# Kernel optimization log

Measured on AMD Instinct MI355X. Metric: run time of the kernel, lower is better.

The kernel has to match this reference:

```python
import jax, jax.numpy as jnp
import numpy as np

N, IN_F, OUT_F, K = 256, 8192, 8320, 16
J = OUT_F - IN_F  # 128


def setup_inputs() -> dict:
    key = jax.random.key(0)
    k1, k2 = jax.random.split(key)
    tensor = jax.random.normal(k1, (N, IN_F), dtype=jnp.float32)
    T = jax.random.normal(k2, (IN_F, J, K), dtype=jnp.float32)
    return {"tensor": tensor, "T": T}


def reference(tensor, T):
    # flatten(start_dim=1) is identity for rank-2 input
    x = tensor.reshape(tensor.shape[0], -1)            # [N, IN_F]
    feats = jnp.einsum('ni,ijk->njk', x, T)            # [N, J, K]
    # pairwise L1 across batch: [N,1,J,K] - [N,J,K] -> [N,N,J,K]
    diff = jnp.abs(feats[:, None, :, :] - feats[None, :, :, :])
    l1 = jnp.sum(diff, axis=3)                         # [N, N, J]
    diversity = jnp.sum(jnp.exp(-l1), axis=1)          # [N, J]
    return jnp.concatenate((x, diversity), axis=1)     # [N, IN_F + J]
```

## Files before the change

kernel.cpp:

```cpp
#include <hip/hip_runtime.h>

typedef unsigned int  u32;
typedef unsigned short u16;

typedef __bf16 bf16x8 __attribute__((ext_vector_type(8)));
typedef float  floatx4 __attribute__((ext_vector_type(4)));

#define N_ROWS 256
#define IN_F   8192
#define OUT_F  8320
#define JDIM   128
#define KDIM   16
#define JK     2048

#define BM     256
#define BN     64
#define BK     64
#define WSTRIDE 72

typedef const __attribute__((address_space(1))) u32 gu32;
typedef __attribute__((address_space(3))) u32 su32;

__device__ __forceinline__ u16 f2bf(float f) {
    u32 u = __float_as_uint(f);
    return (u16)((u + 0x7fffu + ((u >> 16) & 1u)) >> 16);
}
__device__ __forceinline__ float bf2f(u16 h) { return __uint_as_float(((u32)h) << 16); }

__global__ __launch_bounds__(256) void prep_kernel(const float* __restrict__ X,
                                                   float* __restrict__ out,
                                                   u16* __restrict__ Xb)
{
    int t = blockIdx.x * 256 + threadIdx.x;
    float4 v = reinterpret_cast<const float4*>(X)[t];
    int row = t >> 11;
    int c4  = t & 2047;
    reinterpret_cast<float4*>(out + (size_t)row * OUT_F)[c4] = v;
    ushort4 b;
    b.x = f2bf(v.x); b.y = f2bf(v.y); b.z = f2bf(v.z); b.w = f2bf(v.w);
    reinterpret_cast<ushort4*>(Xb)[t] = b;
    if (t < 8192) {
        int r2 = t >> 5, j4 = t & 31;
        reinterpret_cast<float4*>(out + (size_t)r2 * OUT_F + IN_F)[j4] = make_float4(0.f, 0.f, 0.f, 0.f);
    }
}

__global__ __launch_bounds__(256) void gemm_kernel(const u16* __restrict__ Xb,
                                                   const float* __restrict__ W,
                                                   u16* __restrict__ slabs,
                                                   int kchunk)
{
    __shared__ u16 xs[BM * BK];
    __shared__ u16 wt[BN * WSTRIDE];

    const int tid  = threadIdx.x;
    const int lane = tid & 63;
    const int wave = tid >> 6;
    const int c0   = blockIdx.x * BN;
    const int s    = blockIdx.y;
    const int k0base = s * kchunk;

    floatx4 acc[4][4] = {};

    const int xrl = lane >> 3;
    const int xgc = (lane & 7) ^ xrl;
    const int wk  = (tid >> 4) << 2;
    const int wc  = (tid & 15) << 2;

    const float* wptr = W + (size_t)(k0base + wk) * JK + c0 + wc;

    float4 wreg[4];
    #pragma unroll
    for (int r = 0; r < 4; ++r)
        wreg[r] = *(const float4*)(wptr + (size_t)r * JK);

    const int iters = kchunk >> 6;
    for (int it = 0; it < iters; ++it) {
        const int k0 = k0base + it * BK;
        __syncthreads();

        #pragma unroll
        for (int g = 0; g < 8; ++g) {
            int rbase = wave * 64 + g * 8;
            const u16* gp = Xb + (size_t)(rbase + xrl) * IN_F + k0 + xgc * 8;
            u32* lp = (u32*)&xs[rbase * BK];
            __builtin_amdgcn_global_load_lds((gu32*)gp, (su32*)lp, 16, 0, 0);
        }

        {
            const float* wr = (const float*)wreg;
            #pragma unroll
            for (int i = 0; i < 4; ++i) {
                u32 lo = (u32)f2bf(wr[0 * 4 + i]) | ((u32)f2bf(wr[1 * 4 + i]) << 16);
                u32 hi = (u32)f2bf(wr[2 * 4 + i]) | ((u32)f2bf(wr[3 * 4 + i]) << 16);
                uint2 v; v.x = lo; v.y = hi;
                *(uint2*)&wt[(wc + i) * WSTRIDE + wk] = v;
            }
        }
        __syncthreads();

        if (it + 1 < iters) {
            const float* wn = wptr + (size_t)(it + 1) * BK * JK;
            #pragma unroll
            for (int r = 0; r < 4; ++r)
                wreg[r] = *(const float4*)(wn + (size_t)r * JK);
        }

        const int mrow = lane & 15;
        const int q    = lane >> 4;
        #pragma unroll
        for (int h = 0; h < 2; ++h) {
            bf16x8 a[4], b[4];
            #pragma unroll
            for (int rt = 0; rt < 4; ++rt) {
                int rl   = wave * 64 + rt * 16 + mrow;
                int slot = (h * 4 + q) ^ (rl & 7);
                a[rt] = *reinterpret_cast<const bf16x8*>(&xs[rl * BK + slot * 8]);
            }
            #pragma unroll
            for (int ct = 0; ct < 4; ++ct) {
                int col = ct * 16 + mrow;
                b[ct] = *reinterpret_cast<const bf16x8*>(&wt[col * WSTRIDE + (h * 4 + q) * 8]);
            }
            #pragma unroll
            for (int rt = 0; rt < 4; ++rt)
                #pragma unroll
                for (int ct = 0; ct < 4; ++ct)
                    acc[rt][ct] = __builtin_amdgcn_mfma_f32_16x16x32_bf16(a[rt], b[ct], acc[rt][ct], 0, 0, 0);
        }
    }

    const int qe = lane >> 4;
    const int cl = lane & 15;
    u16* sp = slabs + (size_t)s * N_ROWS * JK;
    #pragma unroll
    for (int rt = 0; rt < 4; ++rt)
        #pragma unroll
        for (int ct = 0; ct < 4; ++ct)
            #pragma unroll
            for (int r = 0; r < 4; ++r) {
                int row = wave * 64 + rt * 16 + qe * 4 + r;
                int col = c0 + ct * 16 + cl;
                sp[(size_t)row * JK + col] = f2bf(acc[rt][ct][r]);
            }
}

__global__ __launch_bounds__(256) void reduce_kernel(const u16* __restrict__ slabs,
                                                     float* __restrict__ feats, int S)
{
    int t = blockIdx.x * 256 + threadIdx.x;
    float acc[8] = {};
    for (int s = 0; s < S; ++s) {
        uint4 v = *(const uint4*)(slabs + (size_t)s * N_ROWS * JK + (size_t)t * 8);
        const u16* h = (const u16*)&v;
        #pragma unroll
        for (int e = 0; e < 8; ++e) acc[e] += bf2f(h[e]);
    }
    float4* fp = (float4*)(feats + (size_t)t * 8);
    fp[0] = make_float4(acc[0], acc[1], acc[2], acc[3]);
    fp[1] = make_float4(acc[4], acc[5], acc[6], acc[7]);
}

__global__ __launch_bounds__(256) void pairwise_kernel(const float* __restrict__ feats,
                                                       float* __restrict__ out)
{
    const int j = blockIdx.x;
    const int mq = blockIdx.y;
    const int n = threadIdx.x;

    __shared__ float F[N_ROWS * KDIM];
    const float* fr = feats + (size_t)n * JK + j * KDIM;
    float4 v0 = ((const float4*)fr)[0];
    float4 v1 = ((const float4*)fr)[1];
    float4 v2 = ((const float4*)fr)[2];
    float4 v3 = ((const float4*)fr)[3];
    float4* Fp = (float4*)&F[n * KDIM];
    Fp[0] = v0; Fp[1] = v1; Fp[2] = v2; Fp[3] = v3;
    __syncthreads();

    float f[16] = { v0.x, v0.y, v0.z, v0.w, v1.x, v1.y, v1.z, v1.w,
                    v2.x, v2.y, v2.z, v2.w, v3.x, v3.y, v3.z, v3.w };
    float accum = 0.f;
    const int m0 = mq * 64;
    for (int m = 0; m < 64; ++m) {
        const float* Fm = &F[(m0 + m) * KDIM];
        float l1 = 0.f;
        #pragma unroll
        for (int k = 0; k < 16; ++k) l1 += fabsf(f[k] - Fm[k]);
        accum += exp2f(-1.4426950408889634f * l1);
    }
    atomicAdd(&out[(size_t)n * OUT_F + IN_F + j], accum);
}

extern "C" void kernel_launch(void* const* d_in, const int* in_sizes, int n_in,
                              void* d_out, int out_size, void* d_ws, size_t ws_size,
                              hipStream_t stream)
{
    const float* X = (const float*)d_in[0];
    const float* T = (const float*)d_in[1];
    float* out = (float*)d_out;

    float* feats = (float*)d_ws;
    u16*   Xb    = (u16*)((char*)d_ws + (2u << 20));
    u16*   slabs = (u16*)((char*)d_ws + (6u << 20));

    int S = 16;
    if (ws_size < (6u << 20) + (size_t)16 * N_ROWS * JK * 2) S = 8;
    if (ws_size < (6u << 20) + (size_t)8  * N_ROWS * JK * 2) S = 4;
    int kchunk = IN_F / S;

    prep_kernel<<<2048, 256, 0, stream>>>(X, out, Xb);
    gemm_kernel<<<dim3(JK / BN, S), 256, 0, stream>>>(Xb, T, slabs, kchunk);
    reduce_kernel<<<256, 256, 0, stream>>>(slabs, feats, S);
    pairwise_kernel<<<dim3(JDIM, 4), 256, 0, stream>>>(feats, out);
}
```

Baseline: 139.0 us.

## Stage whole W K-slab in LDS once and stream X operands directly from global

The GEMM kernel now converts and stores the block's entire 512-deep slab of W into shared memory in a single prologue with double-buffered register loads. The main loop then has no barriers and reads the X fragments directly from global memory into registers, prefetching one step ahead, instead of staging X through LDS every 64-K iteration. This removes the per-iteration syncthreads and LDS staging of X. In exchange, X is read from global memory non-coalesced and is fetched redundantly by every column block, which depends on cache hits. The split count is also fixed at 16 slabs, and the fallback for a smaller workspace is dropped.

```diff
diff --git a/kernel.cpp b/kernel.cpp
--- a/kernel.cpp
+++ b/kernel.cpp
@@ -13,13 +13,10 @@
 #define KDIM   16
 #define JK     2048
 
-#define BM     256
-#define BN     64
-#define BK     64
-#define WSTRIDE 72
-
-typedef const __attribute__((address_space(1))) u32 gu32;
-typedef __attribute__((address_space(3))) u32 su32;
+#define BN      64
+#define KSLAB   512
+#define NSLAB   16
+#define WSTRIDE 520
 
 __device__ __forceinline__ u16 f2bf(float f) {
     u32 u = __float_as_uint(f);
@@ -47,10 +44,8 @@
 
 __global__ __launch_bounds__(256) void gemm_kernel(const u16* __restrict__ Xb,
                                                    const float* __restrict__ W,
-                                                   u16* __restrict__ slabs,
-                                                   int kchunk)
-{
-    __shared__ u16 xs[BM * BK];
+                                                   u16* __restrict__ slabs)
+{
     __shared__ u16 wt[BN * WSTRIDE];
 
     const int tid  = threadIdx.x;
@@ -58,76 +53,74 @@
     const int wave = tid >> 6;
     const int c0   = blockIdx.x * BN;
     const int s    = blockIdx.y;
-    const int k0base = s * kchunk;
+    const int k0   = s * KSLAB;
+
+    {
+        const int wc4 = (tid & 15) << 2;
+        const int wk4 = (tid >> 4) << 2;
+        const float* wp0 = W + (size_t)(k0 + wk4) * JK + c0 + wc4;
+
+        float4 wr[2][4];
+        #pragma unroll
+        for (int r = 0; r < 4; ++r) wr[0][r] = *(const float4*)(wp0 + (size_t)r * JK);
+        #pragma unroll
+        for (int r = 0; r < 4; ++r) wr[1][r] = *(const float4*)(wp0 + (size_t)(64 + r) * JK);
+
+        #pragma unroll
+        for (int p = 0; p < 8; ++p) {
+            float4* cur = wr[p & 1];
+            u32 pk[4][2];
+            #pragma unroll
+            for (int i = 0; i < 4; ++i) {
+                const float* c = (const float*)cur;
+                pk[i][0] = (u32)f2bf(c[0 * 4 + i]) | ((u32)f2bf(c[1 * 4 + i]) << 16);
+                pk[i][1] = (u32)f2bf(c[2 * 4 + i]) | ((u32)f2bf(c[3 * 4 + i]) << 16);
+            }
+            if (p + 2 < 8) {
+                const float* wn = wp0 + (size_t)(p + 2) * 64 * JK;
+                #pragma unroll
+                for (int r = 0; r < 4; ++r) cur[r] = *(const float4*)(wn + (size_t)r * JK);
+            }
+            #pragma unroll
+            for (int i = 0; i < 4; ++i)
+                *(uint2*)&wt[(wc4 + i) * WSTRIDE + p * 64 + wk4] = *(uint2*)pk[i];
+        }
+    }
+    __syncthreads();
+
+    const int mrow = lane & 15;
+    const int q    = lane >> 4;
 
     floatx4 acc[4][4] = {};
 
-    const int xrl = lane >> 3;
-    const int xgc = (lane & 7) ^ xrl;
-    const int wk  = (tid >> 4) << 2;
-    const int wc  = (tid & 15) << 2;
-
-    const float* wptr = W + (size_t)(k0base + wk) * JK + c0 + wc;
-
-    float4 wreg[4];
+    const u16* arow[4];
     #pragma unroll
-    for (int r = 0; r < 4; ++r)
-        wreg[r] = *(const float4*)(wptr + (size_t)r * JK);
-
-    const int iters = kchunk >> 6;
-    for (int it = 0; it < iters; ++it) {
-        const int k0 = k0base + it * BK;
-        __syncthreads();
-
-        #pragma unroll
-        for (int g = 0; g < 8; ++g) {
-            int rbase = wave * 64 + g * 8;
-            const u16* gp = Xb + (size_t)(rbase + xrl) * IN_F + k0 + xgc * 8;
-            u32* lp = (u32*)&xs[rbase * BK];
-            __builtin_amdgcn_global_load_lds((gu32*)gp, (su32*)lp, 16, 0, 0);
+    for (int rt = 0; rt < 4; ++rt)
+        arow[rt] = Xb + (size_t)(wave * 64 + rt * 16 + mrow) * IN_F + k0 + q * 8;
+
+    bf16x8 a[4], an[4];
+    #pragma unroll
+    for (int rt = 0; rt < 4; ++rt) a[rt] = *(const bf16x8*)(arow[rt]);
+
+    for (int kc = 0; kc < 16; ++kc) {
+        if (kc + 1 < 16) {
+            #pragma unroll
+            for (int rt = 0; rt < 4; ++rt)
+                an[rt] = *(const bf16x8*)(arow[rt] + (kc + 1) * 32);
         }
-
-        {
-            const float* wr = (const float*)wreg;
-            #pragma unroll
-            for (int i = 0; i < 4; ++i) {
-                u32 lo = (u32)f2bf(wr[0 * 4 + i]) | ((u32)f2bf(wr[1 * 4 + i]) << 16);
-                u32 hi = (u32)f2bf(wr[2 * 4 + i]) | ((u32)f2bf(wr[3 * 4 + i]) << 16);
-                uint2 v; v.x = lo; v.y = hi;
-                *(uint2*)&wt[(wc + i) * WSTRIDE + wk] = v;
-            }
+        bf16x8 b[4];
+        #pragma unroll
+        for (int ct = 0; ct < 4; ++ct) {
+            int col = ct * 16 + mrow;
+            b[ct] = *(const bf16x8*)(&wt[col * WSTRIDE + kc * 32 + q * 8]);
         }
-        __syncthreads();
-
-        if (it + 1 < iters) {
-            const float* wn = wptr + (size_t)(it + 1) * BK * JK;
-            #pragma unroll
-            for (int r = 0; r < 4; ++r)
-                wreg[r] = *(const float4*)(wn + (size_t)r * JK);
-        }
-
-        const int mrow = lane & 15;
-        const int q    = lane >> 4;
-        #pragma unroll
-        for (int h = 0; h < 2; ++h) {
-            bf16x8 a[4], b[4];
-            #pragma unroll
-            for (int rt = 0; rt < 4; ++rt) {
-                int rl   = wave * 64 + rt * 16 + mrow;
-                int slot = (h * 4 + q) ^ (rl & 7);
-                a[rt] = *reinterpret_cast<const bf16x8*>(&xs[rl * BK + slot * 8]);
-            }
-            #pragma unroll
-            for (int ct = 0; ct < 4; ++ct) {
-                int col = ct * 16 + mrow;
-                b[ct] = *reinterpret_cast<const bf16x8*>(&wt[col * WSTRIDE + (h * 4 + q) * 8]);
-            }
-            #pragma unroll
-            for (int rt = 0; rt < 4; ++rt)
-                #pragma unroll
-                for (int ct = 0; ct < 4; ++ct)
-                    acc[rt][ct] = __builtin_amdgcn_mfma_f32_16x16x32_bf16(a[rt], b[ct], acc[rt][ct], 0, 0, 0);
-        }
+        #pragma unroll
+        for (int rt = 0; rt < 4; ++rt)
+            #pragma unroll
+            for (int ct = 0; ct < 4; ++ct)
+                acc[rt][ct] = __builtin_amdgcn_mfma_f32_16x16x32_bf16(a[rt], b[ct], acc[rt][ct], 0, 0, 0);
+        #pragma unroll
+        for (int rt = 0; rt < 4; ++rt) a[rt] = an[rt];
     }
 
     const int qe = lane >> 4;
@@ -146,11 +139,11 @@
 }
 
 __global__ __launch_bounds__(256) void reduce_kernel(const u16* __restrict__ slabs,
-                                                     float* __restrict__ feats, int S)
+                                                     float* __restrict__ feats)
 {
     int t = blockIdx.x * 256 + threadIdx.x;
     float acc[8] = {};
-    for (int s = 0; s < S; ++s) {
+    for (int s = 0; s < NSLAB; ++s) {
         uint4 v = *(const uint4*)(slabs + (size_t)s * N_ROWS * JK + (size_t)t * 8);
         const u16* h = (const u16*)&v;
         #pragma unroll
@@ -204,13 +197,8 @@
     u16*   Xb    = (u16*)((char*)d_ws + (2u << 20));
     u16*   slabs = (u16*)((char*)d_ws + (6u << 20));
 
-    int S = 16;
-    if (ws_size < (6u << 20) + (size_t)16 * N_ROWS * JK * 2) S = 8;
-    if (ws_size < (6u << 20) + (size_t)8  * N_ROWS * JK * 2) S = 4;
-    int kchunk = IN_F / S;
-
     prep_kernel<<<2048, 256, 0, stream>>>(X, out, Xb);
-    gemm_kernel<<<dim3(JK / BN, S), 256, 0, stream>>>(Xb, T, slabs, kchunk);
-    reduce_kernel<<<256, 256, 0, stream>>>(slabs, feats, S);
+    gemm_kernel<<<dim3(JK / BN, NSLAB), 256, 0, stream>>>(Xb, T, slabs);
+    reduce_kernel<<<256, 256, 0, stream>>>(slabs, feats);
     pairwise_kernel<<<dim3(JDIM, 4), 256, 0, stream>>>(feats, out);
 }
```

Result: slower. 143.5 us (+3.2%).
